# Kernel tuning notes

Measured on AMD Instinct MI355X. Metric: run time of the kernel, lower is better.

The kernel has to match this reference:

```python
import jax, jax.numpy as jnp
import numpy as np

B, D, O = 16384, 1024, 2048
MU, LAM = 0.9, 0.1


def setup_inputs() -> dict:
    key = jax.random.key(0)
    ks = jax.random.split(key, 16)
    stdv = float(1.0 / np.sqrt(D))
    u = lambda k, shape, s: jax.random.uniform(k, shape, jnp.float32, -s, s)
    return {
        "x": jax.random.normal(ks[0], (B, D), jnp.float32),
        "x_ctx": jax.random.normal(ks[1], (B, D), jnp.float32),
        "classifier": u(ks[2], (O, D), stdv),
        "none_tensor": u(ks[3], (1, D), stdv),
        "ctx_q_w": u(ks[4], (O, D), stdv),
        "ctx_q_b": u(ks[5], (O,), stdv),
        "word_g_w": u(ks[6], (1, D), stdv),
        "word_g_b": u(ks[7], (1,), stdv),
        "tcq_w1": u(ks[8], (D, D), stdv),
        "tcq_b1": u(ks[9], (D,), stdv),
        "tcq_w2": u(ks[10], (O, D), stdv),
        "tcq_b2": u(ks[11], (O,), stdv),
        "history_input": 0.1 * jax.random.normal(ks[12], (O - 1, D), jnp.float32),
        "history_count": jax.random.randint(ks[13], (O - 1,), 0, 10),
        "labels": jax.random.randint(ks[14], (B,), 0, O),
    }


def reference(x, x_ctx, classifier, none_tensor, ctx_q_w, ctx_q_b,
              word_g_w, word_g_b, tcq_w1, tcq_b1, tcq_w2, tcq_b2,
              history_input, history_count, labels):
    mu, lam = MU, LAM
    # ---- update_history (torch.no_grad), vectorized over classes via segment_sum ----
    xs = jax.lax.stop_gradient(x)
    sums = jax.ops.segment_sum(xs, labels, num_segments=O)               # [O, D]
    counts = jax.ops.segment_sum(jnp.ones((B,), jnp.float32), labels, num_segments=O)  # [O]
    has = counts[1:] > 0                                                  # classes 1..O-1
    cls_mean = sums[1:] / jnp.maximum(counts[1:], 1.0)[:, None]
    hist = jnp.where(has[:, None], mu * history_input + cls_mean, history_input)
    cnt = history_count + has.astype(history_count.dtype)
    # ---- generate_substitute (mu < 1 branch) ----
    denom = 1.0 - jnp.power(mu, jnp.maximum(cnt, 1).astype(jnp.float32))[:, None]
    v = hist * (1.0 - mu) / denom                                        # [O-1, D]
    r_sub = jnp.concatenate([none_tensor, v], axis=0)                    # [O, D]
    ctx_logits = x_ctx @ ctx_q_w.T + ctx_q_b                              # [B, O]
    att_logits = jax.nn.gelu(x @ tcq_w1.T + tcq_b1, approximate=False) @ tcq_w2.T + tcq_b2  # [B, O]
    # ---- gated combine + bilinear classifier (training=True path: w uses ctx_logits) ----
    g_word = jax.nn.sigmoid(x @ word_g_w.T + word_g_b)                    # [B, 1]
    w = g_word * jax.nn.sigmoid(ctx_logits)                               # [B, O]
    # logits = sum(((1-w)*x[:,None,:] + w*r_sub) * classifier, -1), collapsed algebraically
    logits = (1.0 - w) * (x @ classifier.T) + w * jnp.einsum('od,od->o', r_sub, classifier)[None, :]
    # ---- losses on labels >= 0 (mask-weighted means, jit-safe) ----
    mask = (labels >= 0).astype(jnp.float32)
    n = jnp.maximum(mask.sum(), 1.0)
    lsm = jax.nn.log_softmax(logits, axis=-1)
    nll = -jnp.take_along_axis(lsm, jnp.maximum(labels, 0)[:, None], axis=1)[:, 0]
    ce = (mask * nll).sum() / n
    mse_row = jnp.mean((ctx_logits - att_logits) ** 2, axis=-1)
    mse = (mask * mse_row).sum() / n
    return (ce + lam * mse, logits)
```

## Files before the change

### kernel.cpp

```cpp
#include <hip/hip_runtime.h>
#include <cstdint>
#include <cstddef>

#define DEV __device__ __forceinline__

typedef __attribute__((ext_vector_type(4))) float f32x4;
typedef __attribute__((ext_vector_type(8))) short bf16x8;
typedef unsigned short ushort_t;
typedef __attribute__((ext_vector_type(8))) unsigned short ushort8;

static constexpr int B_ = 16384, D_ = 1024, O_ = 2048;
static constexpr float LAM_ = 0.1f;

static constexpr size_t WS_XBF   = 0;
static constexpr size_t WS_XCBF  = WS_XBF   + (size_t)B_ * D_ * 2;
static constexpr size_t WS_HBF   = WS_XCBF  + (size_t)B_ * D_ * 2;
static constexpr size_t WS_CLSBF = WS_HBF   + (size_t)B_ * D_ * 2;
static constexpr size_t WS_CTWBF = WS_CLSBF + (size_t)O_ * D_ * 2;
static constexpr size_t WS_W2BF  = WS_CTWBF + (size_t)O_ * D_ * 2;
static constexpr size_t WS_W1BF  = WS_W2BF  + (size_t)O_ * D_ * 2;
static constexpr size_t WS_SMALL = WS_W1BF  + (size_t)D_ * D_ * 2;
static constexpr size_t SM_COUNTS = 0;
static constexpr size_t SM_TSUM   = 8192;
static constexpr size_t SM_MSE    = 16384;
static constexpr size_t SM_ZERO_BYTES = 82176;
static constexpr size_t SM_S      = 82176;
static constexpr size_t SM_GWORD  = 90368;
static constexpr size_t SM_CEROW  = 155904;

DEV float wave_sum(float v) {
  #pragma unroll
  for (int o = 32; o; o >>= 1) v += __shfl_xor(v, o, 64);
  return v;
}

DEV ushort_t f2bf1(float f) {
  union { float f; unsigned u; } c{f};
  unsigned r = c.u + 0x7fffu + ((c.u >> 16) & 1u);
  return (ushort_t)(r >> 16);
}

DEV float sigmoidf(float z) { return 1.0f / (1.0f + expf(-z)); }

DEV void gload_lds16(const ushort_t* g, ushort_t* l) {
  __builtin_amdgcn_global_load_lds((const __attribute__((address_space(1))) void*)g,
                                   (__attribute__((address_space(3))) void*)l, 16, 0, 0);
}

DEV void stage2(const ushort_t* __restrict__ s0, ushort_t* slot, int tid) {
  gload_lds16(s0, slot + tid * 8);
  gload_lds16(s0 + 128 * 1024, slot + (tid + 512) * 8);
}

DEV f32x4 mfma16(bf16x8 a, bf16x8 b, f32x4 c) {
  return __builtin_amdgcn_mfma_f32_16x16x32_bf16(a, b, c, 0, 0, 0);
}

__global__ __launch_bounds__(256) void f2bf_kernel(const float* __restrict__ in,
                                                   ushort_t* __restrict__ out, int n8) {
  int i = blockIdx.x * 256 + threadIdx.x;
  if (i >= n8) return;
  const float4* p = (const float4*)(in + (size_t)i * 8);
  float4 a = p[0], b = p[1];
  ushort8 o;
  o[0] = f2bf1(a.x); o[1] = f2bf1(a.y); o[2] = f2bf1(a.z); o[3] = f2bf1(a.w);
  o[4] = f2bf1(b.x); o[5] = f2bf1(b.y); o[6] = f2bf1(b.z); o[7] = f2bf1(b.w);
  *(ushort8*)(out + (size_t)i * 8) = o;
}

__global__ __launch_bounds__(256) void rowdot_kernel(const float* __restrict__ x,
    const float* __restrict__ cls, const float* __restrict__ wg,
    const float* __restrict__ wgb, const int* __restrict__ labels,
    float* __restrict__ tsum, float* __restrict__ counts, float* __restrict__ g_word) {
  int wave = threadIdx.x >> 6, lane = threadIdx.x & 63;
  int row = blockIdx.x * 4 + wave;
  const float* xr = x + (size_t)row * D_;
  int lab = labels[row];
  const float* cr = cls + (size_t)max(lab, 0) * D_;
  float t = 0.f, g = 0.f;
  #pragma unroll
  for (int j = 0; j < 4; ++j) {
    int d = j * 256 + lane * 4;
    float4 xv = *(const float4*)(xr + d);
    float4 cv = *(const float4*)(cr + d);
    float4 wv = *(const float4*)(wg + d);
    t += xv.x * cv.x + xv.y * cv.y + xv.z * cv.z + xv.w * cv.w;
    g += xv.x * wv.x + xv.y * wv.y + xv.z * wv.z + xv.w * wv.w;
  }
  t = wave_sum(t); g = wave_sum(g);
  if (lane == 0) {
    if (lab >= 0) {
      atomicAdd(&tsum[lab], t);
      atomicAdd(&counts[lab], 1.0f);
    }
    g_word[row] = sigmoidf(g + wgb[0]);
  }
}

__global__ __launch_bounds__(256) void scls_kernel(const float* __restrict__ cls,
    const float* __restrict__ none_t, const float* __restrict__ hist,
    const int* __restrict__ hcnt, const float* __restrict__ counts,
    const float* __restrict__ tsum, float* __restrict__ s) {
  int wave = threadIdx.x >> 6, lane = threadIdx.x & 63;
  int o = blockIdx.x * 4 + wave;
  if (o >= O_) return;
  const float* cr = cls + (size_t)o * D_;
  const float* src = (o == 0) ? none_t : hist + (size_t)(o - 1) * D_;
  float dv = 0.f;
  #pragma unroll
  for (int j = 0; j < 4; ++j) {
    int d = j * 256 + lane * 4;
    float4 a = *(const float4*)(src + d);
    float4 c = *(const float4*)(cr + d);
    dv += a.x * c.x + a.y * c.y + a.z * c.z + a.w * c.w;
  }
  dv = wave_sum(dv);
  if (lane == 0) {
    if (o == 0) { s[0] = dv; }
    else {
      float co = counts[o];
      bool has = co > 0.f;
      int cnt = hcnt[o - 1] + (has ? 1 : 0);
      float denom = 1.f - powf(0.9f, (float)max(cnt, 1));
      float val = has ? (0.9f * dv + tsum[o] / fmaxf(co, 1.f)) : dv;
      s[o] = (0.1f / denom) * val;
    }
  }
}

template<bool S01, bool S23, int W1, int W3>
DEV void tile8(int t, const ushort_t* __restrict__ sA0, const ushort_t* __restrict__ sB0,
               ushort_t* lds, int tid, int aoff, int boff, f32x4 (&acc)[8][4]) {
  const int k0 = 2 * t, k1 = 2 * t + 1;
  const ushort_t* As0 = lds + (k0 & 3) * 8192;
  const ushort_t* Bs0 = lds + 32768 + (k0 & 3) * 8192;
  const ushort_t* As1 = lds + (k1 & 3) * 8192;
  const ushort_t* Bs1 = lds + 32768 + (k1 & 3) * 8192;
  bf16x8 afr[4], bfr[4];
  #pragma unroll
  for (int n = 0; n < 4; n++) bfr[n] = *(const bf16x8*)&Bs0[boff + n * 512];
  #pragma unroll
  for (int m = 0; m < 4; m++) afr[m] = *(const bf16x8*)&As0[aoff + m * 512];
  if constexpr (S01) stage2(sA0 + (size_t)(2 * t + 3) * 32, lds + ((2 * t + 3) & 3) * 8192, tid);
  __builtin_amdgcn_s_barrier();
  __builtin_amdgcn_s_setprio(1);
  #pragma unroll
  for (int m = 0; m < 4; m++)
    #pragma unroll
    for (int n = 0; n < 4; n++) acc[m][n] = mfma16(afr[m], bfr[n], acc[m][n]);
  __builtin_amdgcn_s_setprio(0);
  __builtin_amdgcn_s_barrier();
  #pragma unroll
  for (int m = 0; m < 4; m++) afr[m] = *(const bf16x8*)&As0[aoff + (m + 4) * 512];
  if constexpr (S01) stage2(sB0 + (size_t)(2 * t + 3) * 32, lds + 32768 + ((2 * t + 3) & 3) * 8192, tid);
  __builtin_amdgcn_s_barrier();
  __builtin_amdgcn_s_setprio(1);
  #pragma unroll
  for (int m = 0; m < 4; m++)
    #pragma unroll
    for (int n = 0; n < 4; n++) acc[m + 4][n] = mfma16(afr[m], bfr[n], acc[m + 4][n]);
  __builtin_amdgcn_s_setprio(0);
  if constexpr (W1 == 8) asm volatile("s_waitcnt vmcnt(8)" ::: "memory");
  else if constexpr (W1 == 4) asm volatile("s_waitcnt vmcnt(4)" ::: "memory");
  else if constexpr (W1 == 2) asm volatile("s_waitcnt vmcnt(2)" ::: "memory");
  else if constexpr (W1 == 0) asm volatile("s_waitcnt vmcnt(0)" ::: "memory");
  __builtin_amdgcn_s_barrier();
  #pragma unroll
  for (int n = 0; n < 4; n++) bfr[n] = *(const bf16x8*)&Bs1[boff + n * 512];
  #pragma unroll
  for (int m = 0; m < 4; m++) afr[m] = *(const bf16x8*)&As1[aoff + m * 512];
  if constexpr (S23) stage2(sA0 + (size_t)(2 * t + 4) * 32, lds + ((2 * t + 4) & 3) * 8192, tid);
  __builtin_amdgcn_s_barrier();
  __builtin_amdgcn_s_setprio(1);
  #pragma unroll
  for (int m = 0; m < 4; m++)
    #pragma unroll
    for (int n = 0; n < 4; n++) acc[m][n] = mfma16(afr[m], bfr[n], acc[m][n]);
  __builtin_amdgcn_s_setprio(0);
  __builtin_amdgcn_s_barrier();
  #pragma unroll
  for (int m = 0; m < 4; m++) afr[m] = *(const bf16x8*)&As1[aoff + (m + 4) * 512];
  if constexpr (S23) stage2(sB0 + (size_t)(2 * t + 4) * 32, lds + 32768 + ((2 * t + 4) & 3) * 8192, tid);
  __builtin_amdgcn_s_barrier();
  __builtin_amdgcn_s_setprio(1);
  #pragma unroll
  for (int m = 0; m < 4; m++)
    #pragma unroll
    for (int n = 0; n < 4; n++) acc[m + 4][n] = mfma16(afr[m], bfr[n], acc[m + 4][n]);
  __builtin_amdgcn_s_setprio(0);
  if constexpr (W3 == 8) asm volatile("s_waitcnt vmcnt(8)" ::: "memory");
  else if constexpr (W3 == 4) asm volatile("s_waitcnt vmcnt(4)" ::: "memory");
  else if constexpr (W3 == 2) asm volatile("s_waitcnt vmcnt(2)" ::: "memory");
  else if constexpr (W3 == 0) asm volatile("s_waitcnt vmcnt(0)" ::: "memory");
  __builtin_amdgcn_s_barrier();
}

template<int EPI, int NTSHIFT>
__global__ __launch_bounds__(512, 2) void gemm8_kernel(
    const ushort_t* __restrict__ A, const ushort_t* __restrict__ Bmat,
    const float* __restrict__ bias, float* __restrict__ fout,
    ushort_t* __restrict__ hout, const float* __restrict__ g_word,
    const float* __restrict__ svec, float* __restrict__ mse_row) {
  __shared__ __align__(16) ushort_t lds[65536];
  const int tid = threadIdx.x, lane = tid & 63, wave = tid >> 6;
  const int wr = wave >> 2, wc = wave & 3;
  const int nwg = 64 << NTSHIFT, cpx = nwg >> 3;
  int bid = blockIdx.x;
  int wg = (bid & 7) * cpx + (bid >> 3);
  const int bm = wg >> NTSHIFT, bn = wg & ((1 << NTSHIFT) - 1);
  const int NCOL = 256 << NTSHIFT;
  const int qsrc = (tid & 3) ^ ((tid >> 3) & 3);
  const ushort_t* sA0 = A + ((size_t)bm * 256 + (tid >> 2)) * 1024 + qsrc * 8;
  const ushort_t* sB0 = Bmat + ((size_t)bn * 256 + (tid >> 2)) * 1024 + qsrc * 8;
  const int qrd = (lane >> 4) ^ (((lane & 15) >> 1) & 3);
  const int aoff = (wr * 128 + (lane & 15)) * 32 + qrd * 8;
  const int boff = (wc * 64 + (lane & 15)) * 32 + qrd * 8;
  f32x4 acc[8][4] = {};
  stage2(sA0, lds, tid);
  stage2(sB0, lds + 32768, tid);
  stage2(sA0 + 32, lds + 8192, tid);
  stage2(sB0 + 32, lds + 32768 + 8192, tid);
  stage2(sA0 + 64, lds + 2 * 8192, tid);
  stage2(sB0 + 64, lds + 32768 + 2 * 8192, tid);
  asm volatile("s_waitcnt vmcnt(8)" ::: "memory");
  __builtin_amdgcn_s_barrier();
  for (int t = 0; t < 14; ++t)
    tile8<true, true, 8, 8>(t, sA0, sB0, lds, tid, aoff, boff, acc);
  tile8<true, false, 8, 4>(14, sA0, sB0, lds, tid, aoff, boff, acc);
  tile8<false, false, 0, -1>(15, sA0, sB0, lds, tid, aoff, boff, acc);
  #pragma unroll
  for (int m = 0; m < 8; m++) {
    #pragma unroll
    for (int i = 0; i < 4; i++) {
      int row = bm * 256 + wr * 128 + m * 16 + (lane >> 4) * 4 + i;
      float gw = 0.f, msum = 0.f;
      if constexpr (EPI == 3) gw = g_word[row];
      #pragma unroll
      for (int n = 0; n < 4; n++) {
        int col = bn * 256 + wc * 64 + n * 16 + (lane & 15);
        float v = acc[m][n][i];
        if constexpr (EPI == 0) {
          float z = v + bias[col];
          float gl = 0.5f * z * (1.f + erff(z * 0.70710678118f));
          hout[(size_t)row * 1024 + col] = f2bf1(gl);
        } else if constexpr (EPI == 1) {
          fout[(size_t)row * NCOL + col] = v + bias[col];
        } else if constexpr (EPI == 2) {
          float att = v + bias[col];
          float ctx = fout[(size_t)row * NCOL + col];
          float d = ctx - att;
          msum += d * d;
        } else {
          size_t off = (size_t)row * NCOL + col;
          float ctx = fout[off];
          float w = gw * sigmoidf(ctx);
          fout[off] = (1.f - w) * v + w * svec[col];
        }
      }
      if constexpr (EPI == 2) {
        #pragma unroll
        for (int o = 1; o < 16; o <<= 1) msum += __shfl_xor(msum, o, 64);
        if ((lane & 15) == 0) atomicAdd(&mse_row[row], msum);
      }
    }
  }
}

__global__ __launch_bounds__(256) void ce_kernel(const float* __restrict__ logits,
    const int* __restrict__ labels, float* __restrict__ ce_row) {
  int row = blockIdx.x, t = threadIdx.x, lane = t & 63, wave = t >> 6;
  const float* lr = logits + (size_t)row * O_;
  float v[8];
  float m = -INFINITY;
  #pragma unroll
  for (int j = 0; j < 8; j++) { v[j] = lr[t + j * 256]; m = fmaxf(m, v[j]); }
  #pragma unroll
  for (int o = 32; o; o >>= 1) m = fmaxf(m, __shfl_xor(m, o, 64));
  __shared__ float red[8];
  if (lane == 0) red[wave] = m;
  __syncthreads();
  m = fmaxf(fmaxf(red[0], red[1]), fmaxf(red[2], red[3]));
  float se = 0.f;
  #pragma unroll
  for (int j = 0; j < 8; j++) se += expf(v[j] - m);
  se = wave_sum(se);
  if (lane == 0) red[4 + wave] = se;
  __syncthreads();
  if (t == 0) {
    float bs = red[4] + red[5] + red[6] + red[7];
    int lab = labels[row];
    float nll = 0.f;
    if (lab >= 0) nll = -(lr[lab] - m - logf(bs));
    ce_row[row] = nll;
  }
}

__global__ __launch_bounds__(256) void finalize_kernel(const float* __restrict__ ce_row,
    const float* __restrict__ mse_row, const int* __restrict__ labels,
    float* __restrict__ out0) {
  int t = threadIdx.x, lane = t & 63, wave = t >> 6;
  float sn = 0.f, sm = 0.f, sc = 0.f;
  for (int i = t; i < B_; i += 256) {
    if (labels[i] >= 0) { sn += ce_row[i]; sm += mse_row[i]; sc += 1.f; }
  }
  sn = wave_sum(sn); sm = wave_sum(sm); sc = wave_sum(sc);
  __shared__ float r0[4], r1[4], r2[4];
  if (lane == 0) { r0[wave] = sn; r1[wave] = sm; r2[wave] = sc; }
  __syncthreads();
  if (t == 0) {
    float a = r0[0] + r0[1] + r0[2] + r0[3];
    float b = r1[0] + r1[1] + r1[2] + r1[3];
    float c = r2[0] + r2[1] + r2[2] + r2[3];
    out0[0] = (a + LAM_ * (b / (float)O_)) / fmaxf(c, 1.f);
  }
}

extern "C" void kernel_launch(void* const* d_in, const int* in_sizes, int n_in,
                              void* d_out, int out_size, void* d_ws, size_t ws_size,
                              hipStream_t stream) {
  const float* x        = (const float*)d_in[0];
  const float* x_ctx    = (const float*)d_in[1];
  const float* cls      = (const float*)d_in[2];
  const float* none_t   = (const float*)d_in[3];
  const float* ctx_q_w  = (const float*)d_in[4];
  const float* ctx_q_b  = (const float*)d_in[5];
  const float* word_g_w = (const float*)d_in[6];
  const float* word_g_b = (const float*)d_in[7];
  const float* w1       = (const float*)d_in[8];
  const float* b1       = (const float*)d_in[9];
  const float* w2       = (const float*)d_in[10];
  const float* b2       = (const float*)d_in[11];
  const float* hist     = (const float*)d_in[12];
  const int*   hcnt     = (const int*)d_in[13];
  const int*   labels   = (const int*)d_in[14];

  float* out  = (float*)d_out;
  float* out1 = out + 1;
  char* ws = (char*)d_ws;

  ushort_t* xbf   = (ushort_t*)(ws + WS_XBF);
  ushort_t* xcbf  = (ushort_t*)(ws + WS_XCBF);
  ushort_t* hbf   = (ushort_t*)(ws + WS_HBF);
  ushort_t* clsbf = (ushort_t*)(ws + WS_CLSBF);
  ushort_t* ctwbf = (ushort_t*)(ws + WS_CTWBF);
  ushort_t* w2bf  = (ushort_t*)(ws + WS_W2BF);
  ushort_t* w1bf  = (ushort_t*)(ws + WS_W1BF);
  float* counts   = (float*)(ws + WS_SMALL + SM_COUNTS);
  float* tsum     = (float*)(ws + WS_SMALL + SM_TSUM);
  float* mse_row  = (float*)(ws + WS_SMALL + SM_MSE);
  float* s        = (float*)(ws + WS_SMALL + SM_S);
  float* g_word   = (float*)(ws + WS_SMALL + SM_GWORD);
  float* ce_row   = (float*)(ws + WS_SMALL + SM_CEROW);

  hipMemsetAsync(ws + WS_SMALL, 0, SM_ZERO_BYTES, stream);

  f2bf_kernel<<<8192, 256, 0, stream>>>(x, xbf, B_ * D_ / 8);
  f2bf_kernel<<<8192, 256, 0, stream>>>(x_ctx, xcbf, B_ * D_ / 8);
  f2bf_kernel<<<1024, 256, 0, stream>>>(cls, clsbf, O_ * D_ / 8);
  f2bf_kernel<<<1024, 256, 0, stream>>>(ctx_q_w, ctwbf, O_ * D_ / 8);
  f2bf_kernel<<<1024, 256, 0, stream>>>(w2, w2bf, O_ * D_ / 8);
  f2bf_kernel<<<512, 256, 0, stream>>>(w1, w1bf, D_ * D_ / 8);

  rowdot_kernel<<<B_ / 4, 256, 0, stream>>>(x, cls, word_g_w, word_g_b, labels,
                                            tsum, counts, g_word);
  scls_kernel<<<O_ / 4, 256, 0, stream>>>(cls, none_t, hist, hcnt, counts, tsum, s);

  gemm8_kernel<0, 2><<<64 * 4, 512, 0, stream>>>(xbf, w1bf, b1, nullptr, hbf,
                                                 nullptr, nullptr, nullptr);
  gemm8_kernel<1, 3><<<64 * 8, 512, 0, stream>>>(xcbf, ctwbf, ctx_q_b, out1, nullptr,
                                                 nullptr, nullptr, nullptr);
  gemm8_kernel<2, 3><<<64 * 8, 512, 0, stream>>>(hbf, w2bf, b2, out1, nullptr,
                                                 nullptr, nullptr, mse_row);
  gemm8_kernel<3, 3><<<64 * 8, 512, 0, stream>>>(xbf, clsbf, nullptr, out1, nullptr,
                                                 g_word, s, nullptr);

  ce_kernel<<<B_, 256, 0, stream>>>(out1, labels, ce_row);
  finalize_kernel<<<1, 256, 0, stream>>>(ce_row, mse_row, labels, out);
}
```

Baseline: 464.2 us.

## Fuse softmax partials into logits GEMM epilogue and store ctx logits as bf16

The logits GEMM epilogue now computes a per-row partial max and sum-exp for each 256-column tile and writes them out, so a small finalize kernel combines the partials instead of re-reading the full logits matrix in a separate softmax pass. When the workspace is large enough, ctx logits are stored as bf16 in scratch rather than fp32 in the output, which halves their re-read traffic in the later kernels. The MSE GEMM is replaced by a simpler 128x128-tile kernel without a multi-stage pipeline. Risks are a slower unpipelined MSE GEMM, bf16 rounding of the ctx logits that feed the sigmoid and the MSE, and extra workspace use.

```diff
diff --git a/kernel.cpp b/kernel.cpp
--- a/kernel.cpp
+++ b/kernel.cpp
@@ -27,6 +27,10 @@
 static constexpr size_t SM_S      = 82176;
 static constexpr size_t SM_GWORD  = 90368;
 static constexpr size_t SM_CEROW  = 155904;
+static constexpr size_t SM_PMAX   = 262144;
+static constexpr size_t SM_PSUM   = 262144 + 524288;
+static constexpr size_t WS_CTXBF  = WS_SMALL + 2 * 1024 * 1024;
+static constexpr size_t WS_NEED_BIG = WS_CTXBF + (size_t)B_ * O_ * 2;
 
 DEV float wave_sum(float v) {
   #pragma unroll
@@ -40,6 +44,11 @@
   return (ushort_t)(r >> 16);
 }
 
+DEV float bf2f(ushort_t u) {
+  union { unsigned u; float f; } c{(unsigned)u << 16};
+  return c.f;
+}
+
 DEV float sigmoidf(float z) { return 1.0f / (1.0f + expf(-z)); }
 
 DEV void gload_lds16(const ushort_t* g, ushort_t* l) {
@@ -52,8 +61,22 @@
   gload_lds16(s0 + 128 * 1024, slot + (tid + 512) * 8);
 }
 
+DEV void stage128s(const ushort_t* __restrict__ src, ushort_t* lds_, int tid) {
+  int c0 = tid, c1 = tid + 256;
+  int q0 = (c0 & 3) ^ ((c0 >> 3) & 3);
+  int q1 = (c1 & 3) ^ ((c1 >> 3) & 3);
+  gload_lds16(src + (size_t)(c0 >> 2) * 1024 + q0 * 8, lds_ + c0 * 8);
+  gload_lds16(src + (size_t)(c1 >> 2) * 1024 + q1 * 8, lds_ + c1 * 8);
+}
+
 DEV f32x4 mfma16(bf16x8 a, bf16x8 b, f32x4 c) {
   return __builtin_amdgcn_mfma_f32_16x16x32_bf16(a, b, c, 0, 0, 0);
+}
+
+template<int N> DEV void wait_vm() {
+  if constexpr (N == 8)      asm volatile("s_waitcnt vmcnt(8)" ::: "memory");
+  else if constexpr (N == 4) asm volatile("s_waitcnt vmcnt(4)" ::: "memory");
+  else if constexpr (N == 0) asm volatile("s_waitcnt vmcnt(0)" ::: "memory");
 }
 
 __global__ __launch_bounds__(256) void f2bf_kernel(const float* __restrict__ in,
@@ -160,10 +183,7 @@
     #pragma unroll
     for (int n = 0; n < 4; n++) acc[m + 4][n] = mfma16(afr[m], bfr[n], acc[m + 4][n]);
   __builtin_amdgcn_s_setprio(0);
-  if constexpr (W1 == 8) asm volatile("s_waitcnt vmcnt(8)" ::: "memory");
-  else if constexpr (W1 == 4) asm volatile("s_waitcnt vmcnt(4)" ::: "memory");
-  else if constexpr (W1 == 2) asm volatile("s_waitcnt vmcnt(2)" ::: "memory");
-  else if constexpr (W1 == 0) asm volatile("s_waitcnt vmcnt(0)" ::: "memory");
+  wait_vm<W1>();
   __builtin_amdgcn_s_barrier();
   #pragma unroll
   for (int n = 0; n < 4; n++) bfr[n] = *(const bf16x8*)&Bs1[boff + n * 512];
@@ -188,19 +208,17 @@
     #pragma unroll
     for (int n = 0; n < 4; n++) acc[m + 4][n] = mfma16(afr[m], bfr[n], acc[m + 4][n]);
   __builtin_amdgcn_s_setprio(0);
-  if constexpr (W3 == 8) asm volatile("s_waitcnt vmcnt(8)" ::: "memory");
-  else if constexpr (W3 == 4) asm volatile("s_waitcnt vmcnt(4)" ::: "memory");
-  else if constexpr (W3 == 2) asm volatile("s_waitcnt vmcnt(2)" ::: "memory");
-  else if constexpr (W3 == 0) asm volatile("s_waitcnt vmcnt(0)" ::: "memory");
-  __builtin_amdgcn_s_barrier();
-}
-
-template<int EPI, int NTSHIFT>
+  wait_vm<W3>();
+  __builtin_amdgcn_s_barrier();
+}
+
+template<int EPI, int NTSHIFT, bool CTXB>
 __global__ __launch_bounds__(512, 2) void gemm8_kernel(
     const ushort_t* __restrict__ A, const ushort_t* __restrict__ Bmat,
     const float* __restrict__ bias, float* __restrict__ fout,
-    ushort_t* __restrict__ hout, const float* __restrict__ g_word,
-    const float* __restrict__ svec, float* __restrict__ mse_row) {
+    ushort_t* __restrict__ hout, ushort_t* __restrict__ ctxbf,
+    const float* __restrict__ g_word, const float* __restrict__ svec,
+    float* __restrict__ pmax, float* __restrict__ psum) {
   __shared__ __align__(16) ushort_t lds[65536];
   const int tid = threadIdx.x, lane = tid & 63, wave = tid >> 6;
   const int wr = wave >> 2, wc = wave & 3;
@@ -222,77 +240,149 @@
   stage2(sB0 + 32, lds + 32768 + 8192, tid);
   stage2(sA0 + 64, lds + 2 * 8192, tid);
   stage2(sB0 + 64, lds + 32768 + 2 * 8192, tid);
-  asm volatile("s_waitcnt vmcnt(8)" ::: "memory");
+  wait_vm<8>();
   __builtin_amdgcn_s_barrier();
   for (int t = 0; t < 14; ++t)
     tile8<true, true, 8, 8>(t, sA0, sB0, lds, tid, aoff, boff, acc);
   tile8<true, false, 8, 4>(14, sA0, sB0, lds, tid, aoff, boff, acc);
   tile8<false, false, 0, -1>(15, sA0, sB0, lds, tid, aoff, boff, acc);
+  float* lred = (float*)lds;
   #pragma unroll
   for (int m = 0; m < 8; m++) {
     #pragma unroll
     for (int i = 0; i < 4; i++) {
-      int row = bm * 256 + wr * 128 + m * 16 + (lane >> 4) * 4 + i;
-      float gw = 0.f, msum = 0.f;
-      if constexpr (EPI == 3) gw = g_word[row];
+      int rloc = wr * 128 + m * 16 + (lane >> 4) * 4 + i;
+      int row = bm * 256 + rloc;
+      if constexpr (EPI == 0 || EPI == 1) {
+        #pragma unroll
+        for (int n = 0; n < 4; n++) {
+          int col = bn * 256 + wc * 64 + n * 16 + (lane & 15);
+          float v = acc[m][n][i] + bias[col];
+          if constexpr (EPI == 0) {
+            float gl = 0.5f * v * (1.f + erff(v * 0.70710678118f));
+            hout[(size_t)row * 1024 + col] = f2bf1(gl);
+          } else if constexpr (CTXB) {
+            ctxbf[(size_t)row * O_ + col] = f2bf1(v);
+          } else {
+            fout[(size_t)row * NCOL + col] = v;
+          }
+        }
+      } else {
+        float gw = g_word[row];
+        float vals[4];
+        float vmax = -INFINITY;
+        #pragma unroll
+        for (int n = 0; n < 4; n++) {
+          int col = bn * 256 + wc * 64 + n * 16 + (lane & 15);
+          size_t off = (size_t)row * NCOL + col;
+          float ctx = CTXB ? bf2f(ctxbf[(size_t)row * O_ + col]) : fout[off];
+          float w = gw * sigmoidf(ctx);
+          float lv = (1.f - w) * acc[m][n][i] + w * svec[col];
+          fout[off] = lv;
+          vals[n] = lv;
+          vmax = fmaxf(vmax, lv);
+        }
+        #pragma unroll
+        for (int o = 1; o < 16; o <<= 1) vmax = fmaxf(vmax, __shfl_xor(vmax, o, 64));
+        float se = 0.f;
+        #pragma unroll
+        for (int n = 0; n < 4; n++) se += expf(vals[n] - vmax);
+        #pragma unroll
+        for (int o = 1; o < 16; o <<= 1) se += __shfl_xor(se, o, 64);
+        if ((lane & 15) == 0) {
+          lred[(wc * 256 + rloc) * 2] = vmax;
+          lred[(wc * 256 + rloc) * 2 + 1] = se;
+        }
+      }
+    }
+  }
+  if constexpr (EPI == 3) {
+    __syncthreads();
+    if (tid < 256) {
+      float M = -INFINITY;
+      #pragma unroll
+      for (int j = 0; j < 4; j++) M = fmaxf(M, lred[(j * 256 + tid) * 2]);
+      float S = 0.f;
+      #pragma unroll
+      for (int j = 0; j < 4; j++)
+        S += lred[(j * 256 + tid) * 2 + 1] * expf(lred[(j * 256 + tid) * 2] - M);
+      size_t gi = (size_t)bn * B_ + bm * 256 + tid;
+      pmax[gi] = M;
+      psum[gi] = S;
+    }
+  }
+}
+
+template<bool CTXB>
+__global__ __launch_bounds__(256, 3) void gemm128_att(
+    const ushort_t* __restrict__ A, const ushort_t* __restrict__ Bmat,
+    const float* __restrict__ bias, const float* __restrict__ fout,
+    const ushort_t* __restrict__ ctxbf, float* __restrict__ mse_row) {
+  __shared__ __align__(16) ushort_t As[128 * 32], Bs[128 * 32];
+  const int tid = threadIdx.x, lane = tid & 63, wave = tid >> 6;
+  const int wr = wave >> 1, wc = wave & 1;
+  int bid = blockIdx.x;
+  int group = bid >> 7, within = bid & 127;
+  int bm = group * 8 + (within & 7);
+  int bn = within >> 3;
+  f32x4 acc[4][4] = {};
+  const ushort_t* Ap = A + (size_t)bm * 128 * 1024;
+  const ushort_t* Bp = Bmat + (size_t)bn * 128 * 1024;
+  const int r = lane & 15;
+  const int qrd8 = ((lane >> 4) ^ ((r >> 1) & 3)) * 8;
+  for (int k0 = 0; k0 < 1024; k0 += 32) {
+    stage128s(Ap + k0, As, tid);
+    stage128s(Bp + k0, Bs, tid);
+    asm volatile("s_waitcnt vmcnt(0)" ::: "memory");
+    __builtin_amdgcn_s_barrier();
+    bf16x8 af[4], bf[4];
+    #pragma unroll
+    for (int m = 0; m < 4; m++) af[m] = *(const bf16x8*)&As[(wr * 64 + m * 16 + r) * 32 + qrd8];
+    #pragma unroll
+    for (int n = 0; n < 4; n++) bf[n] = *(const bf16x8*)&Bs[(wc * 64 + n * 16 + r) * 32 + qrd8];
+    #pragma unroll
+    for (int m = 0; m < 4; m++)
+      #pragma unroll
+      for (int n = 0; n < 4; n++) acc[m][n] = mfma16(af[m], bf[n], acc[m][n]);
+    __builtin_amdgcn_s_barrier();
+  }
+  #pragma unroll
+  for (int m = 0; m < 4; m++) {
+    #pragma unroll
+    for (int i = 0; i < 4; i++) {
+      int row = bm * 128 + wr * 64 + m * 16 + (lane >> 4) * 4 + i;
+      float msum = 0.f;
       #pragma unroll
       for (int n = 0; n < 4; n++) {
-        int col = bn * 256 + wc * 64 + n * 16 + (lane & 15);
-        float v = acc[m][n][i];
-        if constexpr (EPI == 0) {
-          float z = v + bias[col];
-          float gl = 0.5f * z * (1.f + erff(z * 0.70710678118f));
-          hout[(size_t)row * 1024 + col] = f2bf1(gl);
-        } else if constexpr (EPI == 1) {
-          fout[(size_t)row * NCOL + col] = v + bias[col];
-        } else if constexpr (EPI == 2) {
-          float att = v + bias[col];
-          float ctx = fout[(size_t)row * NCOL + col];
-          float d = ctx - att;
-          msum += d * d;
-        } else {
-          size_t off = (size_t)row * NCOL + col;
-          float ctx = fout[off];
-          float w = gw * sigmoidf(ctx);
-          fout[off] = (1.f - w) * v + w * svec[col];
-        }
+        int col = bn * 128 + wc * 64 + n * 16 + (lane & 15);
+        float att = acc[m][n][i] + bias[col];
+        float ctx = CTXB ? bf2f(ctxbf[(size_t)row * O_ + col])
+                         : fout[(size_t)row * O_ + col];
+        float d = ctx - att;
+        msum += d * d;
       }
-      if constexpr (EPI == 2) {
-        #pragma unroll
-        for (int o = 1; o < 16; o <<= 1) msum += __shfl_xor(msum, o, 64);
-        if ((lane & 15) == 0) atomicAdd(&mse_row[row], msum);
-      }
+      #pragma unroll
+      for (int o = 1; o < 16; o <<= 1) msum += __shfl_xor(msum, o, 64);
+      if ((lane & 15) == 0) atomicAdd(&mse_row[row], msum);
     }
   }
 }
 
-__global__ __launch_bounds__(256) void ce_kernel(const float* __restrict__ logits,
+__global__ __launch_bounds__(256) void ce_fin_kernel(const float* __restrict__ logits,
+    const float* __restrict__ pmax, const float* __restrict__ psum,
     const int* __restrict__ labels, float* __restrict__ ce_row) {
-  int row = blockIdx.x, t = threadIdx.x, lane = t & 63, wave = t >> 6;
-  const float* lr = logits + (size_t)row * O_;
-  float v[8];
-  float m = -INFINITY;
-  #pragma unroll
-  for (int j = 0; j < 8; j++) { v[j] = lr[t + j * 256]; m = fmaxf(m, v[j]); }
-  #pragma unroll
-  for (int o = 32; o; o >>= 1) m = fmaxf(m, __shfl_xor(m, o, 64));
-  __shared__ float red[8];
-  if (lane == 0) red[wave] = m;
-  __syncthreads();
-  m = fmaxf(fmaxf(red[0], red[1]), fmaxf(red[2], red[3]));
-  float se = 0.f;
-  #pragma unroll
-  for (int j = 0; j < 8; j++) se += expf(v[j] - m);
-  se = wave_sum(se);
-  if (lane == 0) red[4 + wave] = se;
-  __syncthreads();
-  if (t == 0) {
-    float bs = red[4] + red[5] + red[6] + red[7];
-    int lab = labels[row];
-    float nll = 0.f;
-    if (lab >= 0) nll = -(lr[lab] - m - logf(bs));
-    ce_row[row] = nll;
-  }
+  int row = blockIdx.x * 256 + threadIdx.x;
+  float M = -INFINITY;
+  #pragma unroll
+  for (int j = 0; j < 8; j++) M = fmaxf(M, pmax[(size_t)j * B_ + row]);
+  float S = 0.f;
+  #pragma unroll
+  for (int j = 0; j < 8; j++)
+    S += psum[(size_t)j * B_ + row] * expf(pmax[(size_t)j * B_ + row] - M);
+  int lab = labels[row];
+  float nll = 0.f;
+  if (lab >= 0) nll = -(logits[(size_t)row * O_ + lab] - M - logf(S));
+  ce_row[row] = nll;
 }
 
 __global__ __launch_bounds__(256) void finalize_kernel(const float* __restrict__ ce_row,
@@ -351,6 +441,10 @@
   float* s        = (float*)(ws + WS_SMALL + SM_S);
   float* g_word   = (float*)(ws + WS_SMALL + SM_GWORD);
   float* ce_row   = (float*)(ws + WS_SMALL + SM_CEROW);
+  float* pmax     = (float*)(ws + WS_SMALL + SM_PMAX);
+  float* psum     = (float*)(ws + WS_SMALL + SM_PSUM);
+  ushort_t* ctxbf = (ushort_t*)(ws + WS_CTXBF);
+  const bool big  = ws_size >= WS_NEED_BIG;
 
   hipMemsetAsync(ws + WS_SMALL, 0, SM_ZERO_BYTES, stream);
 
@@ -365,15 +459,30 @@
                                             tsum, counts, g_word);
   scls_kernel<<<O_ / 4, 256, 0, stream>>>(cls, none_t, hist, hcnt, counts, tsum, s);
 
-  gemm8_kernel<0, 2><<<64 * 4, 512, 0, stream>>>(xbf, w1bf, b1, nullptr, hbf,
-                                                 nullptr, nullptr, nullptr);
-  gemm8_kernel<1, 3><<<64 * 8, 512, 0, stream>>>(xcbf, ctwbf, ctx_q_b, out1, nullptr,
-                                                 nullptr, nullptr, nullptr);
-  gemm8_kernel<2, 3><<<64 * 8, 512, 0, stream>>>(hbf, w2bf, b2, out1, nullptr,
-                                                 nullptr, nullptr, mse_row);
-  gemm8_kernel<3, 3><<<64 * 8, 512, 0, stream>>>(xbf, clsbf, nullptr, out1, nullptr,
-                                                 g_word, s, nullptr);
-
-  ce_kernel<<<B_, 256, 0, stream>>>(out1, labels, ce_row);
+  gemm8_kernel<0, 2, false><<<256, 512, 0, stream>>>(xbf, w1bf, b1, nullptr, hbf,
+                                                     nullptr, nullptr, nullptr,
+                                                     nullptr, nullptr);
+  if (big)
+    gemm8_kernel<1, 3, true><<<512, 512, 0, stream>>>(xcbf, ctwbf, ctx_q_b, out1,
+                                                      nullptr, ctxbf, nullptr, nullptr,
+                                                      nullptr, nullptr);
+  else
+    gemm8_kernel<1, 3, false><<<512, 512, 0, stream>>>(xcbf, ctwbf, ctx_q_b, out1,
+                                                       nullptr, nullptr, nullptr, nullptr,
+                                                       nullptr, nullptr);
+  if (big)
+    gemm128_att<true><<<2048, 256, 0, stream>>>(hbf, w2bf, b2, out1, ctxbf, mse_row);
+  else
+    gemm128_att<false><<<2048, 256, 0, stream>>>(hbf, w2bf, b2, out1, nullptr, mse_row);
+  if (big)
+    gemm8_kernel<3, 3, true><<<512, 512, 0, stream>>>(xbf, clsbf, nullptr, out1,
+                                                      nullptr, ctxbf, g_word, s,
+                                                      pmax, psum);
+  else
+    gemm8_kernel<3, 3, false><<<512, 512, 0, stream>>>(xbf, clsbf, nullptr, out1,
+                                                       nullptr, nullptr, g_word, s,
+                                                       pmax, psum);
+
+  ce_fin_kernel<<<B_ / 256, 256, 0, stream>>>(out1, pmax, psum, labels, ce_row);
   finalize_kernel<<<1, 256, 0, stream>>>(ce_row, mse_row, labels, out);
 }
```

Result: no change. 460.5 us (-0.8%).
